# Performance work log

Hardware: AMD Instinct MI355X
Metric: run time of the kernel (lower is better)

## Reference

```python
import jax, jax.numpy as jnp
import numpy as np
import math

B, S, HID = 1, 256, 1024
H, KV, D = 16, 8, 64
N_REP = H // KV


def rotate_half(x):
    x1, x2 = x[..., : x.shape[-1] // 2], x[..., x.shape[-1] // 2 :]
    return jnp.concatenate((-x2, x1), axis=-1)


def setup_inputs() -> dict:
    key = jax.random.key(0)
    ks = jax.random.split(key, 6)
    hidden_states = jax.random.normal(ks[0], (B, S, HID), dtype=jnp.float32)
    # RoPE cos/sin, shape (B, S, D)
    inv_freq = 1.0 / (10000.0 ** (np.arange(0, D, 2, dtype=np.float32) / D))
    freqs = np.arange(S, dtype=np.float32)[:, None] * inv_freq[None, :]  # (S, D/2)
    emb = np.concatenate([freqs, freqs], axis=-1)  # (S, D)
    cos = jnp.broadcast_to(jnp.cos(emb)[None], (B, S, D)).astype(jnp.float32)
    sin = jnp.broadcast_to(jnp.sin(emb)[None], (B, S, D)).astype(jnp.float32)
    # additive causal mask (B,1,S,S)
    neg = jnp.finfo(jnp.float32).min
    causal = jnp.where(jnp.tril(jnp.ones((S, S), dtype=bool)), 0.0, neg)
    attention_mask = jnp.broadcast_to(causal[None, None], (B, 1, S, S)).astype(jnp.float32)
    sc = 0.02
    Wq = jax.random.normal(ks[1], (HID, H * D), dtype=jnp.float32) * sc
    Wk = jax.random.normal(ks[2], (HID, KV * D), dtype=jnp.float32) * sc
    Wv = jax.random.normal(ks[3], (HID, KV * D), dtype=jnp.float32) * sc
    Wo = jax.random.normal(ks[4], (H * D, HID), dtype=jnp.float32) * sc
    return dict(hidden_states=hidden_states, cos=cos, sin=sin,
                attention_mask=attention_mask, Wq=Wq, Wk=Wk, Wv=Wv, Wo=Wo)


def reference(hidden_states, cos, sin, attention_mask, Wq, Wk, Wv, Wo):
    b, s, _ = hidden_states.shape
    scale = 1.0 / math.sqrt(D)
    # projections -> (B, heads, S, D)
    q = (hidden_states @ Wq).reshape(b, s, H, D).transpose(0, 2, 1, 3)
    k = (hidden_states @ Wk).reshape(b, s, KV, D).transpose(0, 2, 1, 3)
    v = (hidden_states @ Wv).reshape(b, s, KV, D).transpose(0, 2, 1, 3)
    # RoPE (cos/sin broadcast over head dim, unsqueeze_dim=1)
    c, sn = cos[:, None, :, :], sin[:, None, :, :]
    q = q * c + rotate_half(q) * sn
    k = k * c + rotate_half(k) * sn
    # repeat kv heads (repeat_interleave over head axis)
    k = jnp.repeat(k, N_REP, axis=1)
    v = jnp.repeat(v, N_REP, axis=1)
    # standard attention logits + mask
    attn_weights = jnp.einsum('bhsd,bhtd->bhst', q, k) * scale + attention_mask
    # per-dim outer product delta: (B,H,D,S,S)
    delta = jnp.einsum('bhsd,bhtd->bhdst', q, k)
    diff = (attn_weights[:, :, None, :, :] - delta) * scale
    p_diff = jax.nn.softmax(diff.astype(jnp.float32), axis=-1)
    p = jax.nn.softmax(attn_weights.astype(jnp.float32), axis=-1)
    # qk importance per (head, dim), flattened to (H*D,)
    qk_importance = ((p_diff - p[:, :, None, :, :]) ** 2).sum(axis=(-2, -1)).sum(axis=0).reshape(-1)
    # attention output
    attn_out = jnp.einsum('bhst,bhtd->bshd', p, v).reshape(b, s, H * D)
    v_importance = jnp.abs(attn_out).sum(axis=(0, 1))
    out = attn_out @ Wo
    o_importance = v_importance  # original computes |attn_output_o| identically
    return out, p, qk_importance, v_importance, o_importance
```

## Files before the change

### kernel.cpp

```cpp
#include <hip/hip_runtime.h>
#include <math.h>

#define SCALE 0.125f
#define LOG2E 1.44269504088896340736f

typedef short short8 __attribute__((ext_vector_type(8)));
typedef float floatx4 __attribute__((ext_vector_type(4)));

static __device__ __forceinline__ ushort f2bf(float x) {
  uint32_t b = __float_as_uint(x);
  uint32_t r = (b + 0x7FFFu + ((b >> 16) & 1u)) >> 16;
  return (ushort)r;
}
static __device__ __forceinline__ float bf2f(ushort u) {
  return __uint_as_float(((uint32_t)u) << 16);
}

__global__ __launch_bounds__(256) void gemm_qkv_kernel(
    const float* __restrict__ X, const float* __restrict__ Wq,
    const float* __restrict__ Wk, const float* __restrict__ Wv,
    float* __restrict__ Cp) {
  __shared__ ushort As[4096];
  __shared__ ushort Bs[4096];
  char* Asc = (char*)As;
  char* Bsc = (char*)Bs;
  const int bx = blockIdx.x;
  const int ks = bx >> 7;
  const int tile = bx & 127;
  const int tile_n = tile & 31, tile_m = tile >> 5;
  const int n0 = tile_n * 64, m0 = tile_m * 64;
  const float* Bp; int ldb, bc0;
  if (n0 < 1024)      { Bp = Wq; ldb = 1024; bc0 = n0; }
  else if (n0 < 1536) { Bp = Wk; ldb = 512;  bc0 = n0 - 1024; }
  else                { Bp = Wv; ldb = 512;  bc0 = n0 - 1536; }
  const int t = threadIdx.x;
  const int arow = t >> 4, acg = t & 15;
  const int bng = t & 15;
  const int kbeg = ks * 256;
  float4 ra[4], rb0[2], rb1[2];
  auto LOAD = [&](int k0) {
    #pragma unroll
    for (int i = 0; i < 4; ++i)
      ra[i] = *reinterpret_cast<const float4*>(X + (size_t)(m0 + arow + 16 * i) * 1024 + k0 + acg * 4);
    #pragma unroll
    for (int i = 0; i < 2; ++i) {
      int k = 2 * ((t >> 4) + 16 * i);
      rb0[i] = *reinterpret_cast<const float4*>(Bp + (size_t)(k0 + k) * ldb + bc0 + bng * 4);
      rb1[i] = *reinterpret_cast<const float4*>(Bp + (size_t)(k0 + k + 1) * ldb + bc0 + bng * 4);
    }
  };
  LOAD(kbeg);
  const int wid = t >> 6, wr = wid >> 1, wc = wid & 1, lane = t & 63;
  const int lr = lane & 15, lk = lane >> 4;
  const int sw = (lr & 7) << 4;
  floatx4 acc[2][2];
  #pragma unroll
  for (int mt = 0; mt < 2; ++mt)
    #pragma unroll
    for (int nt = 0; nt < 2; ++nt)
      acc[mt][nt] = (floatx4){0.f, 0.f, 0.f, 0.f};
  for (int kt = 0; kt < 4; ++kt) {
    #pragma unroll
    for (int i = 0; i < 4; ++i) {
      int row = arow + 16 * i;
      ushort4 w;
      w.x = f2bf(ra[i].x); w.y = f2bf(ra[i].y); w.z = f2bf(ra[i].z); w.w = f2bf(ra[i].w);
      *reinterpret_cast<ushort4*>(Asc + row * 128 + ((acg * 8) ^ ((row & 7) << 4))) = w;
    }
    #pragma unroll
    for (int i = 0; i < 2; ++i) {
      int k = 2 * ((t >> 4) + 16 * i);
      const float* p0 = (const float*)&rb0[i];
      const float* p1 = (const float*)&rb1[i];
      #pragma unroll
      for (int j = 0; j < 4; ++j) {
        int n = bng * 4 + j;
        uint32_t v = (uint32_t)f2bf(p0[j]) | ((uint32_t)f2bf(p1[j]) << 16);
        *reinterpret_cast<uint32_t*>(Bsc + n * 128 + ((k * 2) ^ ((n & 7) << 4))) = v;
      }
    }
    __syncthreads();
    if (kt + 1 < 4) LOAD(kbeg + 64 * (kt + 1));
    #pragma unroll
    for (int kc = 0; kc < 2; ++kc) {
      short8 af[2], bf[2];
      #pragma unroll
      for (int mt = 0; mt < 2; ++mt)
        af[mt] = *reinterpret_cast<const short8*>(
            Asc + (wr * 32 + mt * 16 + lr) * 128 + ((kc * 64 + lk * 16) ^ sw));
      #pragma unroll
      for (int nt = 0; nt < 2; ++nt)
        bf[nt] = *reinterpret_cast<const short8*>(
            Bsc + (wc * 32 + nt * 16 + lr) * 128 + ((kc * 64 + lk * 16) ^ sw));
      #pragma unroll
      for (int mt = 0; mt < 2; ++mt)
        #pragma unroll
        for (int nt = 0; nt < 2; ++nt)
          acc[mt][nt] = __builtin_amdgcn_mfma_f32_16x16x32_bf16(af[mt], bf[nt], acc[mt][nt], 0, 0, 0);
    }
    __syncthreads();
  }
  float* Co = Cp + (size_t)ks * 524288;
  #pragma unroll
  for (int mt = 0; mt < 2; ++mt)
    #pragma unroll
    for (int nt = 0; nt < 2; ++nt)
      #pragma unroll
      for (int r = 0; r < 4; ++r) {
        int row = wr * 32 + mt * 16 + lk * 4 + r;
        int col = wc * 32 + nt * 16 + lr;
        Co[(size_t)(m0 + row) * 2048 + n0 + col] = acc[mt][nt][r];
      }
}

__global__ __launch_bounds__(256) void rope_reduce_kernel(
    const float* __restrict__ Cp, float* __restrict__ QKV,
    const float* __restrict__ cs, const float* __restrict__ sn) {
  int idx = blockIdx.x * 256 + threadIdx.x;
  const float* P0 = Cp;
  const float* P1 = Cp + 524288;
  const float* P2p = Cp + 1048576;
  const float* P3 = Cp + 1572864;
  if (idx < 196608) {
    int dp = idx & 31;
    int head = (idx >> 5) % 24;
    int s = idx / 768;
    int base = s * 2048 + head * 64;
    int a1 = base + dp, a2 = base + dp + 32;
    float x1 = P0[a1] + P1[a1] + P2p[a1] + P3[a1];
    float x2 = P0[a2] + P1[a2] + P2p[a2] + P3[a2];
    float c1 = cs[s * 64 + dp],      s1v = sn[s * 64 + dp];
    float c2 = cs[s * 64 + dp + 32], s2v = sn[s * 64 + dp + 32];
    QKV[a1] = x1 * c1 - x2 * s1v;
    QKV[a2] = x2 * c2 + x1 * s2v;
  } else {
    int i2 = idx - 196608;
    int s = i2 >> 9, c = 1536 + (i2 & 511);
    int a = s * 2048 + c;
    QKV[a] = P0[a] + P1[a] + P2p[a] + P3[a];
  }
}

__global__ __launch_bounds__(512) void pdiff_fused_kernel(
    const float* __restrict__ QKV, float* __restrict__ pOut,
    float* __restrict__ qkpart, float* __restrict__ vpart,
    float* __restrict__ attn_out) {
  __shared__ ushort ksh[16384];
  __shared__ uint32_t kvT[64 * 258];
  __shared__ ushort qsh[1024];
  __shared__ ushort awsh[16][264];
  __shared__ float  epsh[16][260];
  char* kshc = (char*)ksh;
  char* qshc = (char*)qsh;
  const int g = blockIdx.x >> 5;
  const int u = blockIdx.x & 31;
  const int t = threadIdx.x;
  #pragma unroll
  for (int i = 0; i < 8; ++i) {
    int fi = t + i * 512;
    int tt = fi >> 4, c = (fi & 15) * 4;
    float4 kv = *reinterpret_cast<const float4*>(QKV + (size_t)tt * 2048 + 1024 + g * 64 + c);
    float4 vv = *reinterpret_cast<const float4*>(QKV + (size_t)tt * 2048 + 1536 + g * 64 + c);
    ushort4 wk;
    wk.x = f2bf(kv.x); wk.y = f2bf(kv.y); wk.z = f2bf(kv.z); wk.w = f2bf(kv.w);
    *reinterpret_cast<ushort4*>(kshc + tt * 128 + ((c * 2) ^ ((tt & 7) << 4))) = wk;
    kvT[(c + 0) * 258 + tt] = (uint32_t)wk.x | ((uint32_t)f2bf(vv.x) << 16);
    kvT[(c + 1) * 258 + tt] = (uint32_t)wk.y | ((uint32_t)f2bf(vv.y) << 16);
    kvT[(c + 2) * 258 + tt] = (uint32_t)wk.z | ((uint32_t)f2bf(vv.z) << 16);
    kvT[(c + 3) * 258 + tt] = (uint32_t)wk.w | ((uint32_t)f2bf(vv.w) << 16);
  }
  {
    int a = t >> 5;
    int c = (t & 31) * 2;
    int pr = a >> 3, mr = (a >> 2) & 1, jo = a & 3;
    int s = mr ? 255 - (4 * u + jo) : 4 * u + jo;
    int hh = 2 * g + pr;
    float2 qv = *reinterpret_cast<const float2*>(QKV + (size_t)s * 2048 + hh * 64 + c);
    uint32_t pk = (uint32_t)f2bf(qv.x) | ((uint32_t)f2bf(qv.y) << 16);
    *reinterpret_cast<uint32_t*>(qshc + a * 128 + ((c * 2) ^ ((a & 7) << 4))) = pk;
  }
  __syncthreads();
  const int w = t >> 6, lane = t & 63;
  const int lr = lane & 15, lk = lane >> 4;
  const int sw = (lr & 7) << 4;
  const float AWS = SCALE * SCALE * LOG2E;
  #pragma unroll
  for (int q2 = 0; q2 < 2; ++q2) {
    int nt = 2 * w + q2;
    floatx4 acc = (floatx4){0.f, 0.f, 0.f, 0.f};
    #pragma unroll
    for (int kc = 0; kc < 2; ++kc) {
      short8 af = *reinterpret_cast<const short8*>(
          qshc + lr * 128 + ((kc * 64 + lk * 16) ^ sw));
      int tt = nt * 16 + lr;
      short8 bf = *reinterpret_cast<const short8*>(
          kshc + tt * 128 + ((kc * 64 + lk * 16) ^ ((tt & 7) << 4)));
      acc = __builtin_amdgcn_mfma_f32_16x16x32_bf16(af, bf, acc, 0, 0, 0);
    }
    #pragma unroll
    for (int r = 0; r < 4; ++r) {
      int a = lk * 4 + r;
      int pr = a >> 3, mr = (a >> 2) & 1, jo = a & 3;
      int sa = mr ? 255 - (4 * u + jo) : 4 * u + jo;
      int tc = nt * 16 + lr;
      awsh[a][tc] = f2bf((tc <= sa) ? acc[r] * AWS : -1000.0f);
    }
  }
  __syncthreads();
  const int pr = w & 1, jo = w >> 1;
  const int h = 2 * g + pr;
  const int jj = 4 * u + jo;
  #pragma unroll
  for (int r = 0; r < 2; ++r) {
    int a = pr * 8 + r * 4 + jo;
    #pragma unroll
    for (int i = 0; i < 4; ++i) {
      int tc = lane + i * 64;
      epsh[a][tc] = __builtin_amdgcn_exp2f(8.0f * bf2f(awsh[a][tc]));
    }
  }
  float qk_acc = 0.f, v_acc = 0.f;
  for (int r = 0; r < 2; ++r) {
    int a = pr * 8 + r * 4 + jo;
    int s = r ? 255 - jj : jj;
    size_t rowbase = ((size_t)h * 256 + s) * 256;
    float cd2 = (SCALE * LOG2E) * QKV[(size_t)s * 2048 + h * 64 + lane];
    float S1 = 0.f, S2 = 0.f, S3p = 0.f, Sp = 0.f, P2p = 0.f, AVp = 0.f;
    const uint32_t* kvrow = &kvT[lane * 258];
    const ushort* awrow = awsh[a];
    const float* eprow = epsh[a];
    const int nt4 = (s + 4) & ~3;
    #pragma unroll 2
    for (int tb = 0; tb < nt4; tb += 4) {
      uint2 kvA = *reinterpret_cast<const uint2*>(&kvrow[tb]);
      uint2 kvB = *reinterpret_cast<const uint2*>(&kvrow[tb + 2]);
      float4 ep4 = *reinterpret_cast<const float4*>(&eprow[tb]);
      ushort4 aw4 = *reinterpret_cast<const ushort4*>(&awrow[tb]);
      uint32_t kvj[4] = {kvA.x, kvA.y, kvB.x, kvB.y};
      ushort awj[4] = {aw4.x, aw4.y, aw4.z, aw4.w};
      float epj[4] = {ep4.x, ep4.y, ep4.z, ep4.w};
      #pragma unroll
      for (int j = 0; j < 4; ++j) {
        float kf = __uint_as_float(kvj[j] << 16);
        float vf = __uint_as_float(kvj[j] & 0xFFFF0000u);
        float aw = bf2f(awj[j]);
        float e  = __builtin_amdgcn_exp2f(fmaf(-cd2, kf, aw));
        float ep = epj[j];
        S1 += e;
        S2  = fmaf(e, e, S2);
        S3p = fmaf(e, ep, S3p);
        Sp += ep;
        P2p = fmaf(ep, ep, P2p);
        AVp = fmaf(ep, vf, AVp);
      }
    }
    float invS1 = 1.f / S1;
    float invSp = 1.f / Sp;
    qk_acc += S2 * invS1 * invS1 - 2.f * S3p * invS1 * invSp + P2p * invSp * invSp;
    float av = AVp * invSp;
    attn_out[(size_t)s * 1024 + h * 64 + lane] = av;
    v_acc += fabsf(av);
    #pragma unroll
    for (int i = 0; i < 4; ++i) {
      int tc = lane + i * 64;
      pOut[rowbase + tc] = eprow[tc] * invSp;
    }
  }
  qkpart[((size_t)h * 128 + jj) * 64 + lane] = qk_acc;
  vpart [((size_t)h * 128 + jj) * 64 + lane] = v_acc;
}

__global__ __launch_bounds__(256) void gemm_o_tail_kernel(
    const float* __restrict__ A, const float* __restrict__ W,
    const float* __restrict__ qkpart, const float* __restrict__ vpart,
    float* __restrict__ out, float* __restrict__ qkout,
    float* __restrict__ vout, float* __restrict__ oout) {
  __shared__ ushort As[2048];
  __shared__ ushort Bs[2048];
  char* Asc = (char*)As;
  char* Bsc = (char*)Bs;
  const int b = blockIdx.x, t = threadIdx.x;
  if (b < 256) {
    const int tm = b >> 5, tn = b & 31;
    const int m0 = tm * 32, n0 = tn * 32;
    const int arow = t >> 3, aslot = t & 7;
    const int kp = t >> 3, ng = t & 7;
    float4 ra[2], rb0, rb1;
    auto LOAD = [&](int k0) {
      #pragma unroll
      for (int i = 0; i < 2; ++i)
        ra[i] = *reinterpret_cast<const float4*>(A + (size_t)(m0 + arow) * 1024 + k0 + (aslot + 8 * i) * 4);
      rb0 = *reinterpret_cast<const float4*>(W + (size_t)(k0 + 2 * kp) * 1024 + n0 + ng * 4);
      rb1 = *reinterpret_cast<const float4*>(W + (size_t)(k0 + 2 * kp + 1) * 1024 + n0 + ng * 4);
    };
    LOAD(0);
    const int wid = t >> 6, qm = wid >> 1, qn = wid & 1, lane = t & 63;
    const int lr = lane & 15, lk = lane >> 4;
    const int sw = (lr & 7) << 4;
    floatx4 acc = (floatx4){0.f, 0.f, 0.f, 0.f};
    for (int kt = 0; kt < 16; ++kt) {
      #pragma unroll
      for (int i = 0; i < 2; ++i) {
        int c = (aslot + 8 * i) * 4;
        ushort4 wv;
        wv.x = f2bf(ra[i].x); wv.y = f2bf(ra[i].y); wv.z = f2bf(ra[i].z); wv.w = f2bf(ra[i].w);
        *reinterpret_cast<ushort4*>(Asc + arow * 128 + ((c * 2) ^ ((arow & 7) << 4))) = wv;
      }
      {
        const float* p0 = (const float*)&rb0;
        const float* p1 = (const float*)&rb1;
        #pragma unroll
        for (int j = 0; j < 4; ++j) {
          int n = ng * 4 + j;
          uint32_t v = (uint32_t)f2bf(p0[j]) | ((uint32_t)f2bf(p1[j]) << 16);
          *reinterpret_cast<uint32_t*>(Bsc + n * 128 + ((kp * 4) ^ ((n & 7) << 4))) = v;
        }
      }
      __syncthreads();
      if (kt + 1 < 16) LOAD(64 * (kt + 1));
      #pragma unroll
      for (int kc = 0; kc < 2; ++kc) {
        short8 af = *reinterpret_cast<const short8*>(
            Asc + (qm * 16 + lr) * 128 + ((kc * 64 + lk * 16) ^ sw));
        short8 bf = *reinterpret_cast<const short8*>(
            Bsc + (qn * 16 + lr) * 128 + ((kc * 64 + lk * 16) ^ sw));
        acc = __builtin_amdgcn_mfma_f32_16x16x32_bf16(af, bf, acc, 0, 0, 0);
      }
      __syncthreads();
    }
    #pragma unroll
    for (int r = 0; r < 4; ++r) {
      int row = m0 + qm * 16 + lk * 4 + r;
      int col = n0 + qn * 16 + lr;
      out[(size_t)row * 1024 + col] = acc[r];
    }
  } else {
    int idx = (b - 256) * 256 + t;
    if (idx < 1024) {
      int h = idx >> 6, d = idx & 63;
      float sum = 0.f;
      for (int j = 0; j < 128; ++j) sum += qkpart[((size_t)h * 128 + j) * 64 + d];
      qkout[idx] = sum;
    } else {
      int c = idx - 1024;
      int h = c >> 6, d = c & 63;
      float sum = 0.f;
      for (int j = 0; j < 128; ++j) sum += vpart[((size_t)h * 128 + j) * 64 + d];
      vout[c] = sum;
      oout[c] = sum;
    }
  }
}

extern "C" void kernel_launch(void* const* d_in, const int* in_sizes, int n_in,
                              void* d_out, int out_size, void* d_ws, size_t ws_size,
                              hipStream_t stream) {
  const float* X    = (const float*)d_in[0];
  const float* cosp = (const float*)d_in[1];
  const float* sinp = (const float*)d_in[2];
  const float* Wq   = (const float*)d_in[4];
  const float* Wk   = (const float*)d_in[5];
  const float* Wv   = (const float*)d_in[6];
  const float* Wo   = (const float*)d_in[7];

  float* out  = (float*)d_out;
  float* pOut = out + 262144;
  float* qki  = pOut + 1048576;
  float* vi   = qki + 1024;
  float* oi   = vi + 1024;

  float* ws       = (float*)d_ws;
  float* QKV      = ws;
  float* attn_out = ws + 524288;
  float* qkpart   = ws + 786432;
  float* vpart    = ws + 917504;
  float* scratch  = ws + 1048576;

  hipLaunchKernelGGL(gemm_qkv_kernel, dim3(512), dim3(256), 0, stream, X, Wq, Wk, Wv, scratch);
  hipLaunchKernelGGL(rope_reduce_kernel, dim3(1280), dim3(256), 0, stream, scratch, QKV, cosp, sinp);
  hipLaunchKernelGGL(pdiff_fused_kernel, dim3(256), dim3(512), 0, stream, QKV, pOut, qkpart, vpart, attn_out);
  hipLaunchKernelGGL(gemm_o_tail_kernel, dim3(264), dim3(256), 0, stream, attn_out, Wo, qkpart, vpart, out, qki, vi, oi);
}
```

Before: 43.12 us.

## Widen pdiff blocks to 1024 threads, one query row per wave

The fused pdiff kernel now launches 1024 threads per block, so each of its 16 waves handles a single query row instead of two. The MFMA logits tile and the exp precompute are split per wave to match. The v_importance partials are dropped; the tail kernel instead recomputes them by summing |attn_out| over all rows, and the qk partials are now stored per row (256 entries per head). This raises parallelism and shortens each wave's serial loop, at the cost of heavier register pressure under a 1024-thread launch bound and a longer reduction in the tail.

Result: no change. 43.12 us (-0.0%).

```diff
diff --git a/kernel.cpp b/kernel.cpp
--- a/kernel.cpp
+++ b/kernel.cpp
@@ -141,10 +141,9 @@
   }
 }
 
-__global__ __launch_bounds__(512) void pdiff_fused_kernel(
+__global__ __launch_bounds__(1024) void pdiff_fused_kernel(
     const float* __restrict__ QKV, float* __restrict__ pOut,
-    float* __restrict__ qkpart, float* __restrict__ vpart,
-    float* __restrict__ attn_out) {
+    float* __restrict__ qkpart, float* __restrict__ attn_out) {
   __shared__ ushort ksh[16384];
   __shared__ uint32_t kvT[64 * 258];
   __shared__ ushort qsh[1024];
@@ -156,8 +155,8 @@
   const int u = blockIdx.x & 31;
   const int t = threadIdx.x;
   #pragma unroll
-  for (int i = 0; i < 8; ++i) {
-    int fi = t + i * 512;
+  for (int i = 0; i < 4; ++i) {
+    int fi = t + i * 1024;
     int tt = fi >> 4, c = (fi & 15) * 4;
     float4 kv = *reinterpret_cast<const float4*>(QKV + (size_t)tt * 2048 + 1024 + g * 64 + c);
     float4 vv = *reinterpret_cast<const float4*>(QKV + (size_t)tt * 2048 + 1536 + g * 64 + c);
@@ -169,7 +168,7 @@
     kvT[(c + 2) * 258 + tt] = (uint32_t)wk.z | ((uint32_t)f2bf(vv.z) << 16);
     kvT[(c + 3) * 258 + tt] = (uint32_t)wk.w | ((uint32_t)f2bf(vv.w) << 16);
   }
-  {
+  if (t < 512) {
     int a = t >> 5;
     int c = (t & 31) * 2;
     int pr = a >> 3, mr = (a >> 2) & 1, jo = a & 3;
@@ -184,9 +183,8 @@
   const int lr = lane & 15, lk = lane >> 4;
   const int sw = (lr & 7) << 4;
   const float AWS = SCALE * SCALE * LOG2E;
-  #pragma unroll
-  for (int q2 = 0; q2 < 2; ++q2) {
-    int nt = 2 * w + q2;
+  {
+    int nt = w;
     floatx4 acc = (floatx4){0.f, 0.f, 0.f, 0.f};
     #pragma unroll
     for (int kc = 0; kc < 2; ++kc) {
@@ -207,74 +205,64 @@
     }
   }
   __syncthreads();
-  const int pr = w & 1, jo = w >> 1;
+  const int a = w;
+  const int pr = a >> 3, mr = (a >> 2) & 1, jo = a & 3;
   const int h = 2 * g + pr;
-  const int jj = 4 * u + jo;
-  #pragma unroll
-  for (int r = 0; r < 2; ++r) {
-    int a = pr * 8 + r * 4 + jo;
-    #pragma unroll
-    for (int i = 0; i < 4; ++i) {
-      int tc = lane + i * 64;
-      epsh[a][tc] = __builtin_amdgcn_exp2f(8.0f * bf2f(awsh[a][tc]));
-    }
-  }
-  float qk_acc = 0.f, v_acc = 0.f;
-  for (int r = 0; r < 2; ++r) {
-    int a = pr * 8 + r * 4 + jo;
-    int s = r ? 255 - jj : jj;
-    size_t rowbase = ((size_t)h * 256 + s) * 256;
-    float cd2 = (SCALE * LOG2E) * QKV[(size_t)s * 2048 + h * 64 + lane];
-    float S1 = 0.f, S2 = 0.f, S3p = 0.f, Sp = 0.f, P2p = 0.f, AVp = 0.f;
-    const uint32_t* kvrow = &kvT[lane * 258];
-    const ushort* awrow = awsh[a];
-    const float* eprow = epsh[a];
-    const int nt4 = (s + 4) & ~3;
-    #pragma unroll 2
-    for (int tb = 0; tb < nt4; tb += 4) {
-      uint2 kvA = *reinterpret_cast<const uint2*>(&kvrow[tb]);
-      uint2 kvB = *reinterpret_cast<const uint2*>(&kvrow[tb + 2]);
-      float4 ep4 = *reinterpret_cast<const float4*>(&eprow[tb]);
-      ushort4 aw4 = *reinterpret_cast<const ushort4*>(&awrow[tb]);
-      uint32_t kvj[4] = {kvA.x, kvA.y, kvB.x, kvB.y};
-      ushort awj[4] = {aw4.x, aw4.y, aw4.z, aw4.w};
-      float epj[4] = {ep4.x, ep4.y, ep4.z, ep4.w};
-      #pragma unroll
-      for (int j = 0; j < 4; ++j) {
-        float kf = __uint_as_float(kvj[j] << 16);
-        float vf = __uint_as_float(kvj[j] & 0xFFFF0000u);
-        float aw = bf2f(awj[j]);
-        float e  = __builtin_amdgcn_exp2f(fmaf(-cd2, kf, aw));
-        float ep = epj[j];
-        S1 += e;
-        S2  = fmaf(e, e, S2);
-        S3p = fmaf(e, ep, S3p);
-        Sp += ep;
-        P2p = fmaf(ep, ep, P2p);
-        AVp = fmaf(ep, vf, AVp);
-      }
-    }
-    float invS1 = 1.f / S1;
-    float invSp = 1.f / Sp;
-    qk_acc += S2 * invS1 * invS1 - 2.f * S3p * invS1 * invSp + P2p * invSp * invSp;
-    float av = AVp * invSp;
-    attn_out[(size_t)s * 1024 + h * 64 + lane] = av;
-    v_acc += fabsf(av);
-    #pragma unroll
-    for (int i = 0; i < 4; ++i) {
-      int tc = lane + i * 64;
-      pOut[rowbase + tc] = eprow[tc] * invSp;
-    }
-  }
-  qkpart[((size_t)h * 128 + jj) * 64 + lane] = qk_acc;
-  vpart [((size_t)h * 128 + jj) * 64 + lane] = v_acc;
+  const int s = mr ? 255 - (4 * u + jo) : 4 * u + jo;
+  #pragma unroll
+  for (int i = 0; i < 4; ++i) {
+    int tc = lane + i * 64;
+    epsh[a][tc] = __builtin_amdgcn_exp2f(8.0f * bf2f(awsh[a][tc]));
+  }
+  size_t rowbase = ((size_t)h * 256 + s) * 256;
+  float cd2 = (SCALE * LOG2E) * QKV[(size_t)s * 2048 + h * 64 + lane];
+  float S1 = 0.f, S2 = 0.f, S3p = 0.f, Sp = 0.f, P2p = 0.f, AVp = 0.f;
+  const uint32_t* kvrow = &kvT[lane * 258];
+  const ushort* awrow = awsh[a];
+  const float* eprow = epsh[a];
+  const int nt4 = (s + 4) & ~3;
+  #pragma unroll 2
+  for (int tb = 0; tb < nt4; tb += 4) {
+    uint2 kvA = *reinterpret_cast<const uint2*>(&kvrow[tb]);
+    uint2 kvB = *reinterpret_cast<const uint2*>(&kvrow[tb + 2]);
+    float4 ep4 = *reinterpret_cast<const float4*>(&eprow[tb]);
+    ushort4 aw4 = *reinterpret_cast<const ushort4*>(&awrow[tb]);
+    uint32_t kvj[4] = {kvA.x, kvA.y, kvB.x, kvB.y};
+    ushort awj[4] = {aw4.x, aw4.y, aw4.z, aw4.w};
+    float epj[4] = {ep4.x, ep4.y, ep4.z, ep4.w};
+    #pragma unroll
+    for (int j = 0; j < 4; ++j) {
+      float kf = __uint_as_float(kvj[j] << 16);
+      float vf = __uint_as_float(kvj[j] & 0xFFFF0000u);
+      float aw = bf2f(awj[j]);
+      float e  = __builtin_amdgcn_exp2f(fmaf(-cd2, kf, aw));
+      float ep = epj[j];
+      S1 += e;
+      S2  = fmaf(e, e, S2);
+      S3p = fmaf(e, ep, S3p);
+      Sp += ep;
+      P2p = fmaf(ep, ep, P2p);
+      AVp = fmaf(ep, vf, AVp);
+    }
+  }
+  float invS1 = 1.f / S1;
+  float invSp = 1.f / Sp;
+  float qk = S2 * invS1 * invS1 - 2.f * S3p * invS1 * invSp + P2p * invSp * invSp;
+  float av = AVp * invSp;
+  attn_out[(size_t)s * 1024 + h * 64 + lane] = av;
+  #pragma unroll
+  for (int i = 0; i < 4; ++i) {
+    int tc = lane + i * 64;
+    pOut[rowbase + tc] = eprow[tc] * invSp;
+  }
+  qkpart[((size_t)h * 256 + s) * 64 + lane] = qk;
 }
 
 __global__ __launch_bounds__(256) void gemm_o_tail_kernel(
     const float* __restrict__ A, const float* __restrict__ W,
-    const float* __restrict__ qkpart, const float* __restrict__ vpart,
-    float* __restrict__ out, float* __restrict__ qkout,
-    float* __restrict__ vout, float* __restrict__ oout) {
+    const float* __restrict__ qkpart, float* __restrict__ out,
+    float* __restrict__ qkout, float* __restrict__ vout,
+    float* __restrict__ oout) {
   __shared__ ushort As[2048];
   __shared__ ushort Bs[2048];
   char* Asc = (char*)As;
@@ -339,13 +327,12 @@
     if (idx < 1024) {
       int h = idx >> 6, d = idx & 63;
       float sum = 0.f;
-      for (int j = 0; j < 128; ++j) sum += qkpart[((size_t)h * 128 + j) * 64 + d];
+      for (int j = 0; j < 256; ++j) sum += qkpart[((size_t)h * 256 + j) * 64 + d];
       qkout[idx] = sum;
     } else {
       int c = idx - 1024;
-      int h = c >> 6, d = c & 63;
       float sum = 0.f;
-      for (int j = 0; j < 128; ++j) sum += vpart[((size_t)h * 128 + j) * 64 + d];
+      for (int s = 0; s < 256; ++s) sum += fabsf(A[(size_t)s * 1024 + c]);
       vout[c] = sum;
       oout[c] = sum;
     }
@@ -373,11 +360,10 @@
   float* QKV      = ws;
   float* attn_out = ws + 524288;
   float* qkpart   = ws + 786432;
-  float* vpart    = ws + 917504;
   float* scratch  = ws + 1048576;
 
   hipLaunchKernelGGL(gemm_qkv_kernel, dim3(512), dim3(256), 0, stream, X, Wq, Wk, Wv, scratch);
   hipLaunchKernelGGL(rope_reduce_kernel, dim3(1280), dim3(256), 0, stream, scratch, QKV, cosp, sinp);
-  hipLaunchKernelGGL(pdiff_fused_kernel, dim3(256), dim3(512), 0, stream, QKV, pOut, qkpart, vpart, attn_out);
-  hipLaunchKernelGGL(gemm_o_tail_kernel, dim3(264), dim3(256), 0, stream, attn_out, Wo, qkpart, vpart, out, qki, vi, oi);
-}
+  hipLaunchKernelGGL(pdiff_fused_kernel, dim3(256), dim3(1024), 0, stream, QKV, pOut, qkpart, attn_out);
+  hipLaunchKernelGGL(gemm_o_tail_kernel, dim3(264), dim3(256), 0, stream, attn_out, Wo, qkpart, out, qki, vi, oi);
+}
```
